# Kernel tuning notes

Hardware: AMD Instinct MI355X
Metric: run time of the kernel (lower is better)

Reference implementation:

```python
import jax, jax.numpy as jnp
import numpy as np

B, L, D, H, P = 4, 4096, 1024, 8, 4
DPH = D // H


def _grid_sample_row(v, grid):
    """F.grid_sample for a (N, C, 1, Lv) input, bilinear, padding_mode='zeros',
    align_corners=False. v: (N, C, Lv), grid: (N, Lq, P, 2) with (x, y) in last dim.
    Returns (N, C, Lq, P)."""
    N, C, Lv = v.shape
    x = grid[..., 0]
    y = grid[..., 1]
    # unnormalize (align_corners=False): u = ((coord + 1) * size - 1) / 2
    ux = ((x + 1.0) * Lv - 1.0) * 0.5          # width = Lv
    uy = ((y + 1.0) * 1.0 - 1.0) * 0.5         # height = 1
    x0f = jnp.floor(ux)
    wx1 = ux - x0f
    wx0 = 1.0 - wx1
    y0f = jnp.floor(uy)
    wy1 = uy - y0f
    wy0 = 1.0 - wy1
    # only row 0 exists; rows outside contribute zero (padding zeros)
    wy = wy0 * (y0f == 0.0) + wy1 * ((y0f + 1.0) == 0.0)   # (N, Lq, P)
    i0 = x0f.astype(jnp.int32)
    i1 = i0 + 1
    m0 = (i0 >= 0) & (i0 < Lv)
    m1 = (i1 >= 0) & (i1 < Lv)
    i0c = jnp.clip(i0, 0, Lv - 1)
    i1c = jnp.clip(i1, 0, Lv - 1)
    # gather along width per batch element: (C, Lv)[:, (Lq, P)] -> (C, Lq, P)
    v0 = jax.vmap(lambda vv, ii: vv[:, ii])(v, i0c)
    v1 = jax.vmap(lambda vv, ii: vv[:, ii])(v, i1c)
    w0 = (wx0 * m0 * wy)[:, None, :, :]
    w1 = (wx1 * m1 * wy)[:, None, :, :]
    return v0 * w0 + v1 * w1


def setup_inputs() -> dict:
    key = jax.random.key(0)
    ks = jax.random.split(key, 16)
    s = 0.02
    f32 = jnp.float32
    return {
        "query": jax.random.normal(ks[0], (B, L, D), f32),
        "key_in": jax.random.normal(ks[1], (B, L, D), f32),
        "value": jax.random.normal(ks[2], (B, L, D), f32),
        "Wqk": jax.random.normal(ks[3], (D, 2 * D), f32) * s,
        "bqk": jnp.zeros((2 * D,), f32),
        "Wv": jax.random.normal(ks[4], (D, D), f32) * s,
        "bv": jnp.zeros((D,), f32),
        "Woff": jax.random.normal(ks[5], (D, H * P * 2), f32) * s,
        "boff": jax.random.normal(ks[6], (H * P * 2,), f32) * 0.25,
        "Wattn": jax.random.normal(ks[7], (D, H * P), f32) * s,
        "battn": jnp.zeros((H * P,), f32),
        "Wo": jax.random.normal(ks[8], (D, D), f32) * s,
        "bo": jnp.zeros((D,), f32),
    }


def reference(query, key_in, value, Wqk, bqk, Wv, bv, Woff, boff, Wattn, battn, Wo, bo):
    # qk_proj: q, k are computed in the original but never used downstream (dead code)
    qk = query @ Wqk + bqk
    q, k = jnp.split(qk, 2, axis=-1)  # noqa: unused, matches original

    v = value @ Wv + bv                                   # (B, L, D)

    # reference points: x base = linspace[0] = 0, y base = i/(L-1) for query i
    ref_y = jnp.linspace(0.0, 1.0, L)
    ref = jnp.stack([jnp.zeros_like(ref_y), ref_y], axis=-1)   # (L, 2)

    offsets = (query @ Woff + boff).reshape(B, L, H, P, 2)
    attn = jax.nn.softmax((query @ Wattn + battn).reshape(B, L, H, P), axis=-1)

    loc = jnp.clip(ref[None, :, None, None, :] + offsets, 0.0, 1.0)  # (B, L, H, P, 2)

    # value -> (B*H, dph, L)
    vh = v.reshape(B, L, H, DPH).transpose(0, 2, 3, 1).reshape(B * H, DPH, L)
    grid = loc.transpose(0, 2, 1, 3, 4).reshape(B * H, L, P, 2)

    sampled = _grid_sample_row(vh, grid)                  # (B*H, dph, L, P)
    sampled = sampled.reshape(B, H, DPH, L, P)

    aw = attn.transpose(0, 2, 1, 3)[:, :, None, :, :]     # (B, H, 1, L, P)
    out = (sampled * aw).sum(-1)                          # (B, H, dph, L)
    out = out.transpose(0, 3, 1, 2).reshape(B, L, D)
    return out @ Wo + bo
```

## Files before the change

### kernel.cpp

```cpp
#include <hip/hip_runtime.h>

#define L_Q 4096
#define D_MODEL 1024
#define N_B 4
#define N_H 8
#define N_P 4
#define M_ROWS (N_B * L_Q)

typedef float f32x4 __attribute__((ext_vector_type(4)));
typedef __bf16 bf16x8 __attribute__((ext_vector_type(8)));
typedef unsigned short u16x8 __attribute__((ext_vector_type(8)));

__device__ __forceinline__ unsigned short f2bf(float f) {
    unsigned int u = __float_as_uint(f);
    u += 0x7FFFu + ((u >> 16) & 1u);
    return (unsigned short)(u >> 16);
}
__device__ __forceinline__ float bf2f(unsigned short s) {
    return __uint_as_float(((unsigned int)s) << 16);
}

__device__ __forceinline__ void gload_lds16(const void* g, void* l) {
    __builtin_amdgcn_global_load_lds((const __attribute__((address_space(1))) void*)g,
                                     (__attribute__((address_space(3))) void*)l,
                                     16, 0, 0);
}

template <int N> __device__ __forceinline__ void wait_vmc() {
    if constexpr (N == 5)      asm volatile("s_waitcnt vmcnt(5)"  ::: "memory");
    else if constexpr (N == 4) asm volatile("s_waitcnt vmcnt(4)"  ::: "memory");
    else                       asm volatile("s_waitcnt vmcnt(0)"  ::: "memory");
}


__global__ void k_cast_value(const float* __restrict__ in, unsigned short* __restrict__ out, int n4) {
    int i = blockIdx.x * blockDim.x + threadIdx.x;
    const int stride = gridDim.x * blockDim.x;
    for (; i < n4; i += stride) {
        float4 v = ((const float4*)in)[i];
        ushort4 o;
        o.x = f2bf(v.x); o.y = f2bf(v.y); o.z = f2bf(v.z); o.w = f2bf(v.w);
        ((ushort4*)out)[i] = o;
    }
}

__global__ void k_prep_weights(const float* __restrict__ Wv, const float* __restrict__ Wo,
                               const float* __restrict__ Woff, const float* __restrict__ Wattn,
                               unsigned short* __restrict__ WvT, unsigned short* __restrict__ WoT,
                               unsigned short* __restrict__ WcT2) {
    const int n1 = D_MODEL * D_MODEL;
    const int n2 = 2 * n1;
    const int n3 = n2 + 96 * 2048;
    int i = blockIdx.x * blockDim.x + threadIdx.x;
    const int stride = gridDim.x * blockDim.x;
    for (; i < n3; i += stride) {
        if (i < n1) {
            int n = i >> 10, k = i & 1023;
            WvT[i] = f2bf(Wv[k * D_MODEL + n]);
        } else if (i < n2) {
            int j = i - n1;
            int n = j >> 10, k = j & 1023;
            WoT[j] = f2bf(Wo[k * D_MODEL + n]);
        } else {
            int j = i - n2;
            int row = j >> 11;
            int rem = j & 2047;
            int half = rem >> 10;
            int k = rem & 1023;
            float w = (row < 64) ? Woff[k * 64 + row] : Wattn[k * 32 + (row - 64)];
            unsigned short h = f2bf(w);
            WcT2[j] = half ? f2bf(w - bf2f(h)) : h;
        }
    }
}


template <bool OUT_BF16>
__global__ __launch_bounds__(512, 2) void k_gemm256(const unsigned short* __restrict__ A,
                                                    const unsigned short* __restrict__ Bt,
                                                    const float* __restrict__ bias,
                                                    void* __restrict__ Cout) {
    __shared__ __align__(16) unsigned short lds[2][2][2][8192];
    const int tid = threadIdx.x;
    const int w = tid >> 6, lane = tid & 63;
    const int wm = w >> 2, wn = w & 3;

    const int bid = blockIdx.x;
    const int swz = (bid & 7) * 32 + (bid >> 3);
    const int m0 = (swz >> 2) * 256;
    const int n0 = (swz & 3) * 256;

    const int sr = (w << 3) + (lane >> 3);
    const int sc = (lane & 7) ^ ((lane >> 3) & 7);
    const size_t aoff1 = (size_t)(m0 + sr) * 1024 + (size_t)(sc * 8);
    const size_t boff1 = (size_t)(n0 + sr) * 1024 + (size_t)(sc * 8);

    const int fr = lane & 15, kq = lane >> 4;
    const int cs0 = ((kq) ^ (fr & 7)) * 8;
    const int cs1 = ((4 + kq) ^ (fr & 7)) * 8;
    const int arow = (wm * 64 + fr) * 64;
    const int brow = (wn * 32 + fr) * 64;

    f32x4 acc[2][2][4][2];
    const f32x4 zero = {0.f, 0.f, 0.f, 0.f};
#pragma unroll
    for (int qm = 0; qm < 2; ++qm)
#pragma unroll
        for (int qn = 0; qn < 2; ++qn)
#pragma unroll
            for (int i = 0; i < 4; ++i)
#pragma unroll
                for (int j = 0; j < 2; ++j) acc[qm][qn][i][j] = zero;

    bf16x8 af[4][2], bl[2][2], bh[2][2];

#define GSTA(set, half, kt) do {                                                        \
        const unsigned short* g_ = A + aoff1 + (size_t)(half) * 131072 + (size_t)(kt);  \
        unsigned short* d_ = &lds[0][set][half][0] + w * 512;                           \
        gload_lds16(g_, d_);                                                            \
        gload_lds16(g_ + 65536, d_ + 4096);                                             \
    } while (0)

#define GSTB(set, half, kt) do {                                                        \
        const unsigned short* g_ = Bt + boff1 + (size_t)(half) * 131072 + (size_t)(kt); \
        unsigned short* d_ = &lds[1][set][half][0] + w * 512;                           \
        gload_lds16(g_, d_);                                                            \
        gload_lds16(g_ + 65536, d_ + 4096);                                             \
    } while (0)

#define MFMA1(qm, qn, i, j, kk, B_)                                                     \
    acc[qm][qn][i][j] = __builtin_amdgcn_mfma_f32_16x16x32_bf16(                        \
        af[i][kk], B_[j][kk], acc[qm][qn][i][j], 0, 0, 0)

#define LDB4(dst, set, half) do {                                                       \
        const unsigned short* sB_ = &lds[1][set][half][0];                              \
        _Pragma("unroll") for (int j = 0; j < 2; ++j) {                                 \
            dst[j][0] = *(const bf16x8*)(sB_ + brow + j * 1024 + cs0);                  \
            dst[j][1] = *(const bf16x8*)(sB_ + brow + j * 1024 + cs1);                  \
        }                                                                               \
    } while (0)

#define LDA8(set, half) do {                                                            \
        const unsigned short* sA_ = &lds[0][set][half][0];                              \
        _Pragma("unroll") for (int i = 0; i < 4; ++i) {                                 \
            af[i][0] = *(const bf16x8*)(sA_ + arow + i * 1024 + cs0);                   \
            af[i][1] = *(const bf16x8*)(sA_ + arow + i * 1024 + cs1);                   \
        }                                                                               \
    } while (0)

#define MM16(qm, qn, B_) do {                                                           \
        _Pragma("unroll") for (int i = 0; i < 4; ++i) {                                 \
            MFMA1(qm, qn, i, 0, 0, B_); MFMA1(qm, qn, i, 0, 1, B_);                     \
            MFMA1(qm, qn, i, 1, 0, B_); MFMA1(qm, qn, i, 1, 1, B_);                     \
        }                                                                               \
    } while (0)

#define MM16_LDA(qm, qn, B_, setA, halfA) do {                                          \
        const unsigned short* sA_ = &lds[0][setA][halfA][0];                            \
        _Pragma("unroll") for (int i = 0; i < 4; ++i) {                                 \
            MFMA1(qm, qn, i, 0, 0, B_); MFMA1(qm, qn, i, 0, 1, B_);                     \
            MFMA1(qm, qn, i, 1, 0, B_); MFMA1(qm, qn, i, 1, 1, B_);                     \
            af[i][0] = *(const bf16x8*)(sA_ + arow + i * 1024 + cs0);                   \
            af[i][1] = *(const bf16x8*)(sA_ + arow + i * 1024 + cs1);                   \
        }                                                                               \
    } while (0)

#define SGB_MFMA(n) __builtin_amdgcn_sched_group_barrier(0x0008, n, 0)
#define SGB_DSR(n)  __builtin_amdgcn_sched_group_barrier(0x0100, n, 0)
#define PIN_A() do { SGB_DSR(4); SGB_MFMA(16); } while (0)
#define PIN_B() do { SGB_MFMA(4); SGB_DSR(2); SGB_MFMA(4); SGB_DSR(2);                  \
                     SGB_MFMA(4); SGB_DSR(2); SGB_MFMA(4); SGB_DSR(2); } while (0)
#define PIN_D() do { SGB_DSR(4); PIN_B(); } while (0)

#define BAR() do { __builtin_amdgcn_s_barrier(); asm volatile("" ::: "memory"); } while (0)

    GSTA(0, 0, 0);
    GSTB(0, 0, 0);
    GSTB(0, 1, 0);
    GSTA(0, 1, 0);
    wait_vmc<4>();
    BAR();
    LDA8(0, 0); LDB4(bl, 0, 0);

#pragma unroll 1
    for (int it = 0; it < 8; ++it) {
        const int kt = it * 128;
        const int ktn = (kt + 128) & 1023;
        GSTA(1, 0, kt + 64);
        wait_vmc<4>(); BAR();
        __builtin_amdgcn_s_setprio(1);
        LDB4(bh, 0, 1);
        MM16(0, 0, bl);
        PIN_A();
        __builtin_amdgcn_s_setprio(0);
        GSTB(1, 0, kt + 64);
        wait_vmc<4>(); BAR();
        __builtin_amdgcn_s_setprio(1);
        MM16_LDA(0, 1, bh, 0, 1);
        PIN_B();
        __builtin_amdgcn_s_setprio(0);
        GSTB(1, 1, kt + 64);
        BAR();
        __builtin_amdgcn_s_setprio(1);
        MM16(1, 1, bh);
        __builtin_amdgcn_s_setprio(0);
        GSTA(1, 1, kt + 64);
        wait_vmc<4>(); BAR();
        __builtin_amdgcn_s_setprio(1);
        LDB4(bh, 1, 0);
        MM16_LDA(1, 0, bl, 1, 0);
        PIN_D();
        __builtin_amdgcn_s_setprio(0);
        GSTA(0, 0, ktn);
        wait_vmc<4>(); BAR();
        __builtin_amdgcn_s_setprio(1);
        LDB4(bl, 1, 1);
        MM16(0, 0, bh);
        PIN_A();
        __builtin_amdgcn_s_setprio(0);
        GSTB(0, 0, ktn);
        wait_vmc<4>(); BAR();
        __builtin_amdgcn_s_setprio(1);
        MM16_LDA(0, 1, bl, 1, 1);
        PIN_B();
        __builtin_amdgcn_s_setprio(0);
        GSTB(0, 1, ktn);
        BAR();
        __builtin_amdgcn_s_setprio(1);
        MM16(1, 1, bl);
        __builtin_amdgcn_s_setprio(0);
        GSTA(0, 1, ktn);
        wait_vmc<4>(); BAR();
        __builtin_amdgcn_s_setprio(1);
        LDB4(bl, 0, 0);
        MM16_LDA(1, 0, bh, 0, 0);
        PIN_D();
        __builtin_amdgcn_s_setprio(0);
    }
    wait_vmc<0>();

#undef GSTA
#undef GSTB
#undef MFMA1
#undef LDB4
#undef LDA8
#undef MM16
#undef MM16_LDA
#undef SGB_MFMA
#undef SGB_DSR
#undef PIN_A
#undef PIN_B
#undef PIN_D
#undef BAR

#pragma unroll
    for (int qm = 0; qm < 2; ++qm) {
#pragma unroll
        for (int qn = 0; qn < 2; ++qn) {
#pragma unroll
            for (int i = 0; i < 4; ++i) {
#pragma unroll
                for (int j = 0; j < 2; ++j) {
                    const int col = n0 + qn * 128 + wn * 32 + j * 16 + fr;
                    const float bcol = bias[col];
#pragma unroll
                    for (int r = 0; r < 4; ++r) {
                        const int row = m0 + qm * 128 + wm * 64 + i * 16 + kq * 4 + r;
                        const float v = acc[qm][qn][i][j][r] + bcol;
                        if (OUT_BF16)
                            ((unsigned short*)Cout)[(size_t)row * D_MODEL + col] = f2bf(v);
                        else
                            ((float*)Cout)[(size_t)row * D_MODEL + col] = v;
                    }
                }
            }
        }
    }
}


__global__ __launch_bounds__(512, 2) void k_offattn2(const float* __restrict__ query,
                                                     const unsigned short* __restrict__ WcT2,
                                                     const float* __restrict__ boff,
                                                     const float* __restrict__ battn,
                                                     float* __restrict__ C96) {
    __shared__ __align__(16) unsigned short ldsA[2][128 * 64];
    __shared__ __align__(16) unsigned short ldsB[2][192 * 64];
    const int tid = threadIdx.x;
    const int w = tid >> 6, lane = tid & 63;
    const int wm = w >> 1, wn = w & 1;
    const int m0 = blockIdx.x * 64;

    const int ar = tid >> 3;
    const int ac = tid & 7;
    const float* qbase = query + (size_t)(m0 + ar) * 1024 + ac * 8;
    const int aw_hi = ar * 64 + ((ac ^ (ar & 7)) * 8);
    const int aw_lo = (64 + ar) * 64 + ((ac ^ (ar & 7)) * 8);

    const int brl = lane >> 3;
    const int bchk = (lane & 7) ^ (brl & 7);

    const int fr = lane & 15, kq = lane >> 4;
    const int cs0 = ((kq) ^ (fr & 7)) * 8;
    const int cs1 = ((4 + kq) ^ (fr & 7)) * 8;
    const int ahr = (wm * 16 + fr) * 64;
    const int alr = (64 + wm * 16 + fr) * 64;

    f32x4 acc[3];
    const f32x4 zero = {0.f, 0.f, 0.f, 0.f};
#pragma unroll
    for (int j = 0; j < 3; ++j) acc[j] = zero;

#define ALOAD(f0_, f1_, kt_) do {                                                       \
        f0_ = *(const float4*)(qbase + (kt_));                                          \
        f1_ = *(const float4*)(qbase + (kt_) + 4);                                      \
    } while (0)

#define BSTAGE(p_, kt_) do {                                                            \
        _Pragma("unroll") for (int i_ = 0; i_ < 3; ++i_) {                              \
            const int sr_ = i_ * 64 + w * 8 + brl;                                      \
            const unsigned short* g_ = WcT2 + ((sr_ < 96)                               \
                    ? ((size_t)sr_ * 2048 + (size_t)(kt_))                              \
                    : ((size_t)(sr_ - 96) * 2048 + 1024 + (size_t)(kt_)))               \
                    + (size_t)(bchk * 8);                                               \
            gload_lds16(g_, &ldsB[p_][(i_ * 64 + w * 8) * 64]);                         \
        }                                                                               \
    } while (0)

#define AWRITE2(p_, f0_, f1_) do {                                                      \
        u16x8 hi_, lo_;                                                                 \
        const float vv_[8] = {f0_.x, f0_.y, f0_.z, f0_.w, f1_.x, f1_.y, f1_.z, f1_.w};  \
        _Pragma("unroll") for (int e_ = 0; e_ < 8; ++e_) {                              \
            hi_[e_] = f2bf(vv_[e_]);                                                    \
            lo_[e_] = f2bf(vv_[e_] - bf2f(hi_[e_]));                                    \
        }                                                                               \
        *(u16x8*)(&ldsA[p_][aw_hi]) = hi_;                                              \
        *(u16x8*)(&ldsA[p_][aw_lo]) = lo_;                                              \
    } while (0)

#define OMM(p_) do {                                                                    \
        const unsigned short* As_ = &ldsA[p_][0];                                       \
        const unsigned short* Bs_ = &ldsB[p_][0];                                       \
        bf16x8 ah0 = *(const bf16x8*)(As_ + ahr + cs0);                                 \
        bf16x8 ah1 = *(const bf16x8*)(As_ + ahr + cs1);                                 \
        bf16x8 al0 = *(const bf16x8*)(As_ + alr + cs0);                                 \
        bf16x8 al1 = *(const bf16x8*)(As_ + alr + cs1);                                 \
        __builtin_amdgcn_s_setprio(1);                                                  \
        _Pragma("unroll") for (int j = 0; j < 3; ++j) {                                 \
            const int br_ = (wn * 48 + j * 16 + fr) * 64;                               \
            bf16x8 wh0 = *(const bf16x8*)(Bs_ + br_ + cs0);                             \
            bf16x8 wh1 = *(const bf16x8*)(Bs_ + br_ + cs1);                             \
            bf16x8 wl0 = *(const bf16x8*)(Bs_ + 6144 + br_ + cs0);                      \
            bf16x8 wl1 = *(const bf16x8*)(Bs_ + 6144 + br_ + cs1);                      \
            acc[j] = __builtin_amdgcn_mfma_f32_16x16x32_bf16(ah0, wh0, acc[j], 0, 0, 0);\
            acc[j] = __builtin_amdgcn_mfma_f32_16x16x32_bf16(ah1, wh1, acc[j], 0, 0, 0);\
            acc[j] = __builtin_amdgcn_mfma_f32_16x16x32_bf16(ah0, wl0, acc[j], 0, 0, 0);\
            acc[j] = __builtin_amdgcn_mfma_f32_16x16x32_bf16(ah1, wl1, acc[j], 0, 0, 0);\
            acc[j] = __builtin_amdgcn_mfma_f32_16x16x32_bf16(al0, wh0, acc[j], 0, 0, 0);\
            acc[j] = __builtin_amdgcn_mfma_f32_16x16x32_bf16(al1, wh1, acc[j], 0, 0, 0);\
        }                                                                               \
        __builtin_amdgcn_s_setprio(0);                                                  \
    } while (0)

#define OBODY(t_, p_, fc0_, fc1_, fn0_, fn1_) do {                                      \
        if ((t_) < 15) {                                                                \
            ALOAD(fn0_, fn1_, ((t_) + 1) * 64);                                         \
            BSTAGE((p_) ^ 1, ((t_) + 1) * 64);                                          \
            wait_vmc<5>();                                                              \
        } else {                                                                        \
            wait_vmc<0>();                                                              \
        }                                                                               \
        AWRITE2(p_, fc0_, fc1_);                                                        \
        asm volatile("s_waitcnt lgkmcnt(0)" ::: "memory");                              \
        __builtin_amdgcn_s_barrier(); asm volatile("" ::: "memory");                    \
        OMM(p_);                                                                        \
        __builtin_amdgcn_s_barrier(); asm volatile("" ::: "memory");                    \
    } while (0)

    float4 a0A, a1A, a0B, a1B;
    ALOAD(a0A, a1A, 0);
    BSTAGE(0, 0);

#pragma unroll 1
    for (int t2 = 0; t2 < 8; ++t2) {
        const int t = t2 * 2;
        OBODY(t,     0, a0A, a1A, a0B, a1B);
        OBODY(t + 1, 1, a0B, a1B, a0A, a1A);
    }

#undef ALOAD
#undef BSTAGE
#undef AWRITE2
#undef OMM
#undef OBODY

#pragma unroll
    for (int j = 0; j < 3; ++j) {
        const int col = wn * 48 + j * 16 + fr;
        const float bcol = (col < 64) ? boff[col] : battn[col - 64];
#pragma unroll
        for (int r = 0; r < 4; ++r) {
            const int row = m0 + wm * 16 + kq * 4 + r;
            C96[(size_t)row * 96 + col] = acc[j][r] + bcol;
        }
    }
}


__global__ void k_sampler(const float* __restrict__ C96,
                          const unsigned short* __restrict__ vproj,
                          unsigned short* __restrict__ agg) {
    const int row = blockIdx.x;
    const int b = row >> 12;
    const int l = row & (L_Q - 1);
    const int t = threadIdx.x;

    __shared__ float cv[96];
    if (t < 96) cv[t] = C96[(size_t)row * 96 + t];
    __syncthreads();

    const int h = t >> 5;
    const int dd = (t & 31) * 4;
    const float ref_y = (float)l / 4095.0f;

    float lg[4];
#pragma unroll
    for (int p = 0; p < 4; ++p) lg[p] = cv[64 + h * 4 + p];
    const float mx = fmaxf(fmaxf(lg[0], lg[1]), fmaxf(lg[2], lg[3]));
    float ex[4];
    float es = 0.f;
#pragma unroll
    for (int p = 0; p < 4; ++p) { ex[p] = expf(lg[p] - mx); es += ex[p]; }
    const float inv = 1.0f / es;

    float acc0 = 0.f, acc1 = 0.f, acc2 = 0.f, acc3 = 0.f;
#pragma unroll
    for (int p = 0; p < 4; ++p) {
        const float ox = cv[h * 8 + p * 2];
        const float oy = cv[h * 8 + p * 2 + 1];
        const float lx = fminf(fmaxf(ox, 0.0f), 1.0f);
        const float ly = fminf(fmaxf(ref_y + oy, 0.0f), 1.0f);
        const float ux = (lx + 1.0f) * 2048.0f - 0.5f;
        const float wy = 1.0f - ly * 0.5f;
        const float x0f = floorf(ux);
        const int i0 = (int)x0f;
        const int i1 = i0 + 1;
        const float w1 = ux - x0f;
        const float w0 = 1.0f - w1;
        const float aw = ex[p] * inv * wy;
        const float f0 = aw * w0 * ((i0 >= 0 && i0 < L_Q) ? 1.0f : 0.0f);
        const float f1 = aw * w1 * ((i1 >= 0 && i1 < L_Q) ? 1.0f : 0.0f);
        const int i0c = i0 < 0 ? 0 : (i0 > L_Q - 1 ? L_Q - 1 : i0);
        const int i1c = i1 < 0 ? 0 : (i1 > L_Q - 1 ? L_Q - 1 : i1);
        const ushort4 v0 = *(const ushort4*)(vproj + (size_t)(b * L_Q + i0c) * D_MODEL + h * 128 + dd);
        const ushort4 v1 = *(const ushort4*)(vproj + (size_t)(b * L_Q + i1c) * D_MODEL + h * 128 + dd);
        acc0 += f0 * bf2f(v0.x) + f1 * bf2f(v1.x);
        acc1 += f0 * bf2f(v0.y) + f1 * bf2f(v1.y);
        acc2 += f0 * bf2f(v0.z) + f1 * bf2f(v1.z);
        acc3 += f0 * bf2f(v0.w) + f1 * bf2f(v1.w);
    }
    ushort4 o;
    o.x = f2bf(acc0); o.y = f2bf(acc1); o.z = f2bf(acc2); o.w = f2bf(acc3);
    *(ushort4*)(agg + (size_t)row * D_MODEL + t * 4) = o;
}


extern "C" void kernel_launch(void* const* d_in, const int* in_sizes, int n_in,
                              void* d_out, int out_size, void* d_ws, size_t ws_size,
                              hipStream_t stream) {
    const float* query = (const float*)d_in[0];
    const float* value = (const float*)d_in[2];
    const float* Wv    = (const float*)d_in[5];
    const float* bv    = (const float*)d_in[6];
    const float* Woff  = (const float*)d_in[7];
    const float* boff  = (const float*)d_in[8];
    const float* Wattn = (const float*)d_in[9];
    const float* battn = (const float*)d_in[10];
    const float* Wo    = (const float*)d_in[11];
    const float* bo    = (const float*)d_in[12];

    char* ws = (char*)d_ws;
    size_t off = 0;
    auto alloc = [&](size_t bytes) -> char* {
        char* p = ws + off;
        off += (bytes + 255) & ~(size_t)255;
        return p;
    };
    unsigned short* val_bf = (unsigned short*)alloc((size_t)M_ROWS * D_MODEL * 2);
    unsigned short* vproj  = (unsigned short*)alloc((size_t)M_ROWS * D_MODEL * 2);
    unsigned short* agg    = (unsigned short*)alloc((size_t)M_ROWS * D_MODEL * 2);
    float*          C96    = (float*)alloc((size_t)M_ROWS * 96 * 4);
    unsigned short* WvT    = (unsigned short*)alloc((size_t)D_MODEL * D_MODEL * 2);
    unsigned short* WoT    = (unsigned short*)alloc((size_t)D_MODEL * D_MODEL * 2);
    unsigned short* WcT2   = (unsigned short*)alloc((size_t)96 * 2048 * 2);

    const int n4 = M_ROWS * D_MODEL / 4;
    k_cast_value<<<2048, 256, 0, stream>>>(value, val_bf, n4);
    k_prep_weights<<<1024, 256, 0, stream>>>(Wv, Wo, Woff, Wattn, WvT, WoT, WcT2);

    k_gemm256<true><<<256, 512, 0, stream>>>(val_bf, WvT, bv, vproj);

    k_offattn2<<<M_ROWS / 64, 512, 0, stream>>>(query, WcT2, boff, battn, C96);

    k_sampler<<<M_ROWS, 256, 0, stream>>>(C96, vproj, agg);

    k_gemm256<false><<<256, 512, 0, stream>>>(agg, WoT, bo, (float*)d_out);
}
```

Before: 154.1 us.

## Restructure GEMM main loop to prefetch deeper and widen value cast stores

The 256x256 bf16 GEMM main loop is rescheduled. It now keeps three global-to-LDS loads in flight (vmcnt 6), issues each LDS fragment load before a barrier, and separates the MFMA blocks with explicit barriers. This replaces the previous sched_group_barrier interleaving of ds_reads and MFMAs. The value cast kernel is also changed to process 8 floats per thread with 16-byte stores and twice the grid size. The extra barriers and the lost fine-grained interleave could serialize the LDS reads against the MFMAs.

```diff
diff --git a/kernel.cpp b/kernel.cpp
--- a/kernel.cpp
+++ b/kernel.cpp
@@ -27,20 +27,22 @@
 }
 
 template <int N> __device__ __forceinline__ void wait_vmc() {
-    if constexpr (N == 5)      asm volatile("s_waitcnt vmcnt(5)"  ::: "memory");
-    else if constexpr (N == 4) asm volatile("s_waitcnt vmcnt(4)"  ::: "memory");
+    if constexpr (N == 6)      asm volatile("s_waitcnt vmcnt(6)"  ::: "memory");
+    else if constexpr (N == 5) asm volatile("s_waitcnt vmcnt(5)"  ::: "memory");
     else                       asm volatile("s_waitcnt vmcnt(0)"  ::: "memory");
 }
 
 
-__global__ void k_cast_value(const float* __restrict__ in, unsigned short* __restrict__ out, int n4) {
+__global__ void k_cast_value(const float* __restrict__ in, unsigned short* __restrict__ out, int n8) {
     int i = blockIdx.x * blockDim.x + threadIdx.x;
     const int stride = gridDim.x * blockDim.x;
-    for (; i < n4; i += stride) {
-        float4 v = ((const float4*)in)[i];
-        ushort4 o;
-        o.x = f2bf(v.x); o.y = f2bf(v.y); o.z = f2bf(v.z); o.w = f2bf(v.w);
-        ((ushort4*)out)[i] = o;
+    for (; i < n8; i += stride) {
+        float4 a = ((const float4*)in)[2 * i];
+        float4 b = ((const float4*)in)[2 * i + 1];
+        u16x8 o;
+        o[0] = f2bf(a.x); o[1] = f2bf(a.y); o[2] = f2bf(a.z); o[3] = f2bf(a.w);
+        o[4] = f2bf(b.x); o[5] = f2bf(b.y); o[6] = f2bf(b.z); o[7] = f2bf(b.w);
+        ((u16x8*)out)[i] = o;
     }
 }
 
@@ -128,9 +130,13 @@
         gload_lds16(g_ + 65536, d_ + 4096);                                             \
     } while (0)
 
-#define MFMA1(qm, qn, i, j, kk, B_)                                                     \
-    acc[qm][qn][i][j] = __builtin_amdgcn_mfma_f32_16x16x32_bf16(                        \
-        af[i][kk], B_[j][kk], acc[qm][qn][i][j], 0, 0, 0)
+#define LDA8(set, half) do {                                                            \
+        const unsigned short* sA_ = &lds[0][set][half][0];                              \
+        _Pragma("unroll") for (int i = 0; i < 4; ++i) {                                 \
+            af[i][0] = *(const bf16x8*)(sA_ + arow + i * 1024 + cs0);                   \
+            af[i][1] = *(const bf16x8*)(sA_ + arow + i * 1024 + cs1);                   \
+        }                                                                               \
+    } while (0)
 
 #define LDB4(dst, set, half) do {                                                       \
         const unsigned short* sB_ = &lds[1][set][half][0];                              \
@@ -140,117 +146,86 @@
         }                                                                               \
     } while (0)
 
-#define LDA8(set, half) do {                                                            \
-        const unsigned short* sA_ = &lds[0][set][half][0];                              \
-        _Pragma("unroll") for (int i = 0; i < 4; ++i) {                                 \
-            af[i][0] = *(const bf16x8*)(sA_ + arow + i * 1024 + cs0);                   \
-            af[i][1] = *(const bf16x8*)(sA_ + arow + i * 1024 + cs1);                   \
-        }                                                                               \
-    } while (0)
-
 #define MM16(qm, qn, B_) do {                                                           \
-        _Pragma("unroll") for (int i = 0; i < 4; ++i) {                                 \
-            MFMA1(qm, qn, i, 0, 0, B_); MFMA1(qm, qn, i, 0, 1, B_);                     \
-            MFMA1(qm, qn, i, 1, 0, B_); MFMA1(qm, qn, i, 1, 1, B_);                     \
-        }                                                                               \
-    } while (0)
-
-#define MM16_LDA(qm, qn, B_, setA, halfA) do {                                          \
-        const unsigned short* sA_ = &lds[0][setA][halfA][0];                            \
-        _Pragma("unroll") for (int i = 0; i < 4; ++i) {                                 \
-            MFMA1(qm, qn, i, 0, 0, B_); MFMA1(qm, qn, i, 0, 1, B_);                     \
-            MFMA1(qm, qn, i, 1, 0, B_); MFMA1(qm, qn, i, 1, 1, B_);                     \
-            af[i][0] = *(const bf16x8*)(sA_ + arow + i * 1024 + cs0);                   \
-            af[i][1] = *(const bf16x8*)(sA_ + arow + i * 1024 + cs1);                   \
-        }                                                                               \
-    } while (0)
-
-#define SGB_MFMA(n) __builtin_amdgcn_sched_group_barrier(0x0008, n, 0)
-#define SGB_DSR(n)  __builtin_amdgcn_sched_group_barrier(0x0100, n, 0)
-#define PIN_A() do { SGB_DSR(4); SGB_MFMA(16); } while (0)
-#define PIN_B() do { SGB_MFMA(4); SGB_DSR(2); SGB_MFMA(4); SGB_DSR(2);                  \
-                     SGB_MFMA(4); SGB_DSR(2); SGB_MFMA(4); SGB_DSR(2); } while (0)
-#define PIN_D() do { SGB_DSR(4); PIN_B(); } while (0)
-
+        __builtin_amdgcn_s_setprio(1);                                                  \
+        _Pragma("unroll") for (int i = 0; i < 4; ++i)                                   \
+        _Pragma("unroll") for (int j = 0; j < 2; ++j)                                   \
+        _Pragma("unroll") for (int kk = 0; kk < 2; ++kk)                                \
+            acc[qm][qn][i][j] = __builtin_amdgcn_mfma_f32_16x16x32_bf16(                \
+                af[i][kk], B_[j][kk], acc[qm][qn][i][j], 0, 0, 0);                      \
+        __builtin_amdgcn_s_setprio(0);                                                  \
+    } while (0)
+
+#define LGK8() asm volatile("s_waitcnt lgkmcnt(8)" ::: "memory")
 #define BAR() do { __builtin_amdgcn_s_barrier(); asm volatile("" ::: "memory"); } while (0)
 
     GSTA(0, 0, 0);
     GSTB(0, 0, 0);
     GSTB(0, 1, 0);
     GSTA(0, 1, 0);
-    wait_vmc<4>();
+    GSTA(1, 0, 64);
+    GSTB(1, 0, 64);
+    GSTB(1, 1, 64);
+    wait_vmc<6>();
     BAR();
-    LDA8(0, 0); LDB4(bl, 0, 0);
 
 #pragma unroll 1
     for (int it = 0; it < 8; ++it) {
-        const int kt = it * 128;
+        const int kt  = it * 128;
+        const int kA  = kt + 64;
         const int ktn = (kt + 128) & 1023;
-        GSTA(1, 0, kt + 64);
-        wait_vmc<4>(); BAR();
-        __builtin_amdgcn_s_setprio(1);
+        const int kt2 = (kt + 192) & 1023;
+        LDA8(0, 0); LDB4(bl, 0, 0);
+        GSTA(1, 1, kA);
+        LGK8();
+        BAR();
+        MM16(0, 0, bl);
+        BAR();
         LDB4(bh, 0, 1);
+        GSTA(0, 0, ktn);
+        BAR();
+        MM16(0, 1, bh);
+        BAR();
+        LDA8(0, 1);
+        GSTB(0, 0, ktn);
+        BAR();
+        MM16(1, 1, bh);
+        BAR();
+        GSTB(0, 1, ktn);
+        wait_vmc<6>();
+        BAR();
+        MM16(1, 0, bl);
+        BAR();
+        LDA8(1, 0); LDB4(bl, 1, 0);
+        GSTA(0, 1, ktn);
+        LGK8();
+        BAR();
         MM16(0, 0, bl);
-        PIN_A();
-        __builtin_amdgcn_s_setprio(0);
-        GSTB(1, 0, kt + 64);
-        wait_vmc<4>(); BAR();
-        __builtin_amdgcn_s_setprio(1);
-        MM16_LDA(0, 1, bh, 0, 1);
-        PIN_B();
-        __builtin_amdgcn_s_setprio(0);
-        GSTB(1, 1, kt + 64);
-        BAR();
-        __builtin_amdgcn_s_setprio(1);
+        BAR();
+        LDB4(bh, 1, 1);
+        GSTA(1, 0, kt2);
+        BAR();
+        MM16(0, 1, bh);
+        BAR();
+        LDA8(1, 1);
+        GSTB(1, 0, kt2);
+        BAR();
         MM16(1, 1, bh);
-        __builtin_amdgcn_s_setprio(0);
-        GSTA(1, 1, kt + 64);
-        wait_vmc<4>(); BAR();
-        __builtin_amdgcn_s_setprio(1);
-        LDB4(bh, 1, 0);
-        MM16_LDA(1, 0, bl, 1, 0);
-        PIN_D();
-        __builtin_amdgcn_s_setprio(0);
-        GSTA(0, 0, ktn);
-        wait_vmc<4>(); BAR();
-        __builtin_amdgcn_s_setprio(1);
-        LDB4(bl, 1, 1);
-        MM16(0, 0, bh);
-        PIN_A();
-        __builtin_amdgcn_s_setprio(0);
-        GSTB(0, 0, ktn);
-        wait_vmc<4>(); BAR();
-        __builtin_amdgcn_s_setprio(1);
-        MM16_LDA(0, 1, bl, 1, 1);
-        PIN_B();
-        __builtin_amdgcn_s_setprio(0);
-        GSTB(0, 1, ktn);
-        BAR();
-        __builtin_amdgcn_s_setprio(1);
-        MM16(1, 1, bl);
-        __builtin_amdgcn_s_setprio(0);
-        GSTA(0, 1, ktn);
-        wait_vmc<4>(); BAR();
-        __builtin_amdgcn_s_setprio(1);
-        LDB4(bl, 0, 0);
-        MM16_LDA(1, 0, bh, 0, 0);
-        PIN_D();
-        __builtin_amdgcn_s_setprio(0);
+        BAR();
+        GSTB(1, 1, kt2);
+        wait_vmc<6>();
+        BAR();
+        MM16(1, 0, bl);
+        BAR();
     }
     wait_vmc<0>();
 
 #undef GSTA
 #undef GSTB
-#undef MFMA1
+#undef LDA8
 #undef LDB4
-#undef LDA8
 #undef MM16
-#undef MM16_LDA
-#undef SGB_MFMA
-#undef SGB_DSR
-#undef PIN_A
-#undef PIN_B
-#undef PIN_D
+#undef LGK8
 #undef BAR
 
 #pragma unroll
@@ -494,8 +469,8 @@
     unsigned short* WoT    = (unsigned short*)alloc((size_t)D_MODEL * D_MODEL * 2);
     unsigned short* WcT2   = (unsigned short*)alloc((size_t)96 * 2048 * 2);
 
-    const int n4 = M_ROWS * D_MODEL / 4;
-    k_cast_value<<<2048, 256, 0, stream>>>(value, val_bf, n4);
+    const int n8 = M_ROWS * D_MODEL / 8;
+    k_cast_value<<<4096, 256, 0, stream>>>(value, val_bf, n8);
     k_prep_weights<<<1024, 256, 0, stream>>>(Wv, Wo, Woff, Wattn, WvT, WoT, WcT2);
 
     k_gemm256<true><<<256, 512, 0, stream>>>(val_bf, WvT, bv, vproj);
```

Result: no change. 155.8 us (+1.1%).

## Fuse value cast and weight prep into one kernel with LDS-tiled transposes

Applied to the files above, without the earlier changes.

Merges the value fp32→bf16 cast and the weight transpose/cast kernels into a single launch. Block ranges are partitioned by role. The weight transposes now go through a 64x65 padded shared-memory tile, so both the global reads and the writes are coalesced, replacing the old strided scalar reads. The value cast handles 8 elements per thread with 16-byte stores. This removes one launch and the uncoalesced transpose traffic, but the cast now runs on only about 1500 blocks alongside the weight blocks.

```diff
diff --git a/kernel.cpp b/kernel.cpp
--- a/kernel.cpp
+++ b/kernel.cpp
@@ -33,43 +33,88 @@
 }
 
 
-__global__ void k_cast_value(const float* __restrict__ in, unsigned short* __restrict__ out, int n4) {
-    int i = blockIdx.x * blockDim.x + threadIdx.x;
-    const int stride = gridDim.x * blockDim.x;
-    for (; i < n4; i += stride) {
-        float4 v = ((const float4*)in)[i];
-        ushort4 o;
-        o.x = f2bf(v.x); o.y = f2bf(v.y); o.z = f2bf(v.z); o.w = f2bf(v.w);
-        ((ushort4*)out)[i] = o;
-    }
-}
-
-__global__ void k_prep_weights(const float* __restrict__ Wv, const float* __restrict__ Wo,
-                               const float* __restrict__ Woff, const float* __restrict__ Wattn,
-                               unsigned short* __restrict__ WvT, unsigned short* __restrict__ WoT,
-                               unsigned short* __restrict__ WcT2) {
-    const int n1 = D_MODEL * D_MODEL;
-    const int n2 = 2 * n1;
-    const int n3 = n2 + 96 * 2048;
-    int i = blockIdx.x * blockDim.x + threadIdx.x;
-    const int stride = gridDim.x * blockDim.x;
-    for (; i < n3; i += stride) {
-        if (i < n1) {
-            int n = i >> 10, k = i & 1023;
-            WvT[i] = f2bf(Wv[k * D_MODEL + n]);
-        } else if (i < n2) {
-            int j = i - n1;
-            int n = j >> 10, k = j & 1023;
-            WoT[j] = f2bf(Wo[k * D_MODEL + n]);
-        } else {
-            int j = i - n2;
-            int row = j >> 11;
-            int rem = j & 2047;
-            int half = rem >> 10;
-            int k = rem & 1023;
-            float w = (row < 64) ? Woff[k * 64 + row] : Wattn[k * 32 + (row - 64)];
-            unsigned short h = f2bf(w);
-            WcT2[j] = half ? f2bf(w - bf2f(h)) : h;
+__global__ void k_prep(const float* __restrict__ Wv, const float* __restrict__ Wo,
+                       const float* __restrict__ Woff, const float* __restrict__ Wattn,
+                       const float* __restrict__ value,
+                       unsigned short* __restrict__ WvT, unsigned short* __restrict__ WoT,
+                       unsigned short* __restrict__ WcT2, unsigned short* __restrict__ val_bf) {
+    __shared__ float tile[64 * 65];
+    const int bidx = blockIdx.x;
+    const int t = threadIdx.x;
+
+    if (bidx < 512) {
+        const float* W = (bidx < 256) ? Wv : Wo;
+        unsigned short* WT = (bidx < 256) ? WvT : WoT;
+        const int bi = bidx & 255;
+        const int k0 = (bi >> 4) * 64, n0 = (bi & 15) * 64;
+#pragma unroll
+        for (int j = 0; j < 4; ++j) {
+            const int r = j * 16 + (t >> 4);
+            float4 v = *(const float4*)(W + (size_t)(k0 + r) * 1024 + n0 + (t & 15) * 4);
+            float* d = &tile[r * 65 + (t & 15) * 4];
+            d[0] = v.x; d[1] = v.y; d[2] = v.z; d[3] = v.w;
+        }
+        __syncthreads();
+#pragma unroll
+        for (int j = 0; j < 4; ++j) {
+            const int n = j * 16 + (t >> 4);
+            const int kc = (t & 15) * 4;
+            ushort4 o;
+            o.x = f2bf(tile[(kc + 0) * 65 + n]);
+            o.y = f2bf(tile[(kc + 1) * 65 + n]);
+            o.z = f2bf(tile[(kc + 2) * 65 + n]);
+            o.w = f2bf(tile[(kc + 3) * 65 + n]);
+            *(ushort4*)(WT + (size_t)(n0 + n) * 1024 + k0 + kc) = o;
+        }
+    } else if (bidx < 544) {
+        const int bi = bidx - 512;
+        const int k0 = (bi >> 1) * 64;
+        const int ntile = bi & 1;
+        const int n0 = ntile * 64;
+        const int nw = ntile ? 32 : 64;
+        const int ldw = ntile ? 32 : 64;
+        const float* W = ntile ? Wattn : Woff;
+#pragma unroll
+        for (int j = 0; j < 4; ++j) {
+            const int r = j * 16 + (t >> 4);
+            const int c4 = t & 15;
+            if (c4 * 4 < nw) {
+                float4 v = *(const float4*)(W + (size_t)(k0 + r) * ldw + c4 * 4);
+                float* d = &tile[r * 65 + c4 * 4];
+                d[0] = v.x; d[1] = v.y; d[2] = v.z; d[3] = v.w;
+            }
+        }
+        __syncthreads();
+#pragma unroll
+        for (int j = 0; j < 4; ++j) {
+            const int n = j * 16 + (t >> 4);
+            if (n < nw) {
+                const int kc = (t & 15) * 4;
+                ushort4 hi, lo;
+                float f0 = tile[(kc + 0) * 65 + n];
+                float f1 = tile[(kc + 1) * 65 + n];
+                float f2 = tile[(kc + 2) * 65 + n];
+                float f3 = tile[(kc + 3) * 65 + n];
+                hi.x = f2bf(f0); lo.x = f2bf(f0 - bf2f(hi.x));
+                hi.y = f2bf(f1); lo.y = f2bf(f1 - bf2f(hi.y));
+                hi.z = f2bf(f2); lo.z = f2bf(f2 - bf2f(hi.z));
+                hi.w = f2bf(f3); lo.w = f2bf(f3 - bf2f(hi.w));
+                const size_t base = (size_t)(n0 + n) * 2048 + k0 + kc;
+                *(ushort4*)(WcT2 + base) = hi;
+                *(ushort4*)(WcT2 + base + 1024) = lo;
+            }
+        }
+    } else {
+        const int n8 = M_ROWS * D_MODEL / 8;
+        int i = (bidx - 544) * 256 + t;
+        const int stride = (gridDim.x - 544) * 256;
+        for (; i < n8; i += stride) {
+            float4 a = ((const float4*)value)[2 * i];
+            float4 b = ((const float4*)value)[2 * i + 1];
+            u16x8 o;
+            o[0] = f2bf(a.x); o[1] = f2bf(a.y); o[2] = f2bf(a.z); o[3] = f2bf(a.w);
+            o[4] = f2bf(b.x); o[5] = f2bf(b.y); o[6] = f2bf(b.z); o[7] = f2bf(b.w);
+            ((u16x8*)val_bf)[i] = o;
         }
     }
 }
@@ -494,9 +539,7 @@
     unsigned short* WoT    = (unsigned short*)alloc((size_t)D_MODEL * D_MODEL * 2);
     unsigned short* WcT2   = (unsigned short*)alloc((size_t)96 * 2048 * 2);
 
-    const int n4 = M_ROWS * D_MODEL / 4;
-    k_cast_value<<<2048, 256, 0, stream>>>(value, val_bf, n4);
-    k_prep_weights<<<1024, 256, 0, stream>>>(Wv, Wo, Woff, Wattn, WvT, WoT, WcT2);
+    k_prep<<<2048, 256, 0, stream>>>(Wv, Wo, Woff, Wattn, value, WvT, WoT, WcT2, val_bf);
 
     k_gemm256<true><<<256, 512, 0, stream>>>(val_bf, WvT, bv, vproj);
 
```

New measurement: 141.9 us (median of 2 runs). 1.09x faster.
